# Kernel tuning notes

Measured on AMD Instinct MI355X. Metric: run time of the kernel, lower is better.

## Reference

```python
import jax, jax.numpy as jnp
import numpy as np

B, S, D, H, Dh = 2, 1024, 2048, 16, 128
EPS = 1e-6


def setup_inputs() -> dict:
    key = jax.random.key(0)
    ks = jax.random.split(key, 8)
    hidden_states = jax.random.normal(ks[0], (B, S, D), jnp.float32)
    def qweight(k):
        return jax.random.randint(k, (D, D), -127, 128, dtype=jnp.int32)
    wq, wk, wv, wo = qweight(ks[1]), qweight(ks[2]), qweight(ks[3]), qweight(ks[4])
    def scale(k):
        # per-output-channel dequant scale ~ O(1/(127*sqrt(D)))
        return jax.random.uniform(k, (D,), jnp.float32, 0.5, 1.5) / (127.0 * np.sqrt(D))
    wq_s, wk_s, wv_s, wo_s = scale(ks[5]), scale(ks[6]), scale(ks[7]), scale(jax.random.fold_in(key, 99))
    qn_w = jnp.ones((D,), jnp.float32)
    kn_w = jnp.ones((D,), jnp.float32)
    # RoPE tables (rotate-half convention): [S, Dh]
    pos = jnp.arange(S, dtype=jnp.float32)
    inv_freq = 1.0 / (10000.0 ** (jnp.arange(0, Dh, 2, dtype=jnp.float32) / Dh))
    freqs = pos[:, None] * inv_freq[None, :]              # [S, Dh/2]
    cos = jnp.concatenate([jnp.cos(freqs)] * 2, axis=-1)  # [S, Dh]
    sin = jnp.concatenate([jnp.sin(freqs)] * 2, axis=-1)
    lengths = jnp.array([S, 3 * S // 4], dtype=jnp.int32)
    return dict(hidden_states=hidden_states, wq_s=wq_s, wk_s=wk_s, wv_s=wv_s,
                wo_s=wo_s, qn_w=qn_w, kn_w=kn_w, cos=cos, sin=sin,
                wq=wq, wk=wk, wv=wv, wo=wo, lengths=lengths)


def _q8_linear(x, w_int, scale):
    # Q8Linear: int8 weight [out,in] dequantized by per-output-channel scale
    w = w_int.astype(jnp.float32) * scale[:, None]
    return jnp.einsum('bsd,od->bso', x, w)


def _rms_norm(x, w):
    var = jnp.mean(jnp.square(x), axis=-1, keepdims=True)
    return x * jax.lax.rsqrt(var + EPS) * w


def _apply_rope(x, cos, sin):
    # x: [B,S,D] -> per-head rotate-half RoPE -> [B,S,D]
    xh = x.reshape(B, S, H, Dh)
    x1, x2 = jnp.split(xh, 2, axis=-1)
    rot = jnp.concatenate([-x2, x1], axis=-1)
    out = xh * cos[None, :, None, :] + rot * sin[None, :, None, :]
    return out.reshape(B, S, D)


def reference(hidden_states, wq_s, wk_s, wv_s, wo_s, qn_w, kn_w, cos, sin,
              wq, wk, wv, wo, lengths):
    q = _rms_norm(_q8_linear(hidden_states, wq, wq_s), qn_w)
    k = _rms_norm(_q8_linear(hidden_states, wk, wk_s), kn_w)
    v = _q8_linear(hidden_states, wv, wv_s)
    q = _apply_rope(q, cos, sin)
    k = _apply_rope(k, cos, sin)
    # [B,S,D] -> [B,H,S,Dh]
    q = q.reshape(B, S, H, Dh).transpose(0, 2, 1, 3)
    k = k.reshape(B, S, H, Dh).transpose(0, 2, 1, 3)
    v = v.reshape(B, S, H, Dh).transpose(0, 2, 1, 3)
    # length mask -> additive bias [B,1,1,S]
    positions = jnp.arange(S)
    valid = positions[None, :] < lengths[:, None]
    bias = jnp.where(valid, 0.0, -jnp.inf).astype(jnp.float32)[:, None, None, :]
    scores = jnp.einsum('bhqd,bhkd->bhqk', q, k) / np.sqrt(Dh) + bias
    probs = jax.nn.softmax(scores, axis=-1)
    attn = jnp.einsum('bhqk,bhkd->bhqd', probs, v)
    attn = attn.transpose(0, 2, 1, 3).reshape(B, S, D)
    out = _q8_linear(attn, wo, wo_s)
    return out
```

## Files before the change

### kernel.cpp

```cpp
#include <hip/hip_runtime.h>
#include <stdint.h>

typedef __bf16 bf16;
typedef bf16 bf16x8 __attribute__((ext_vector_type(8)));
typedef bf16 bf16x4 __attribute__((ext_vector_type(4)));
typedef float f32x4 __attribute__((ext_vector_type(4)));

#define B_   2
#define S_   1024
#define D_   2048
#define H_   16
#define DH_  128
#define M_   (B_*S_)
#define EPSF 1e-6f

__device__ __forceinline__ void gload_lds16(const void* g, void* l) {
    __builtin_amdgcn_global_load_lds(
        (const __attribute__((address_space(1))) void*)g,
        (__attribute__((address_space(3))) void*)l,
        16, 0, 0);
}

struct ConvArgs {
    const void* s[5];
    bf16* d[5];
};

__global__ __launch_bounds__(256) void conv_all(ConvArgs a, int n) {
    const int z = blockIdx.y;
    const int i = (blockIdx.x * 256 + threadIdx.x) * 8;
    if (i + 8 > n) return;
    bf16x8 o;
    if (z == 0) {
        const float* src = (const float*)a.s[0];
        float4 v0 = *(const float4*)(src + i);
        float4 v1 = *(const float4*)(src + i + 4);
        o[0] = (bf16)v0.x; o[1] = (bf16)v0.y; o[2] = (bf16)v0.z; o[3] = (bf16)v0.w;
        o[4] = (bf16)v1.x; o[5] = (bf16)v1.y; o[6] = (bf16)v1.z; o[7] = (bf16)v1.w;
    } else {
        const int* src = (const int*)a.s[z];
        int4 v0 = *(const int4*)(src + i);
        int4 v1 = *(const int4*)(src + i + 4);
        o[0] = (bf16)(float)v0.x; o[1] = (bf16)(float)v0.y;
        o[2] = (bf16)(float)v0.z; o[3] = (bf16)(float)v0.w;
        o[4] = (bf16)(float)v1.x; o[5] = (bf16)(float)v1.y;
        o[6] = (bf16)(float)v1.z; o[7] = (bf16)(float)v1.w;
    }
    *(bf16x8*)(a.d[z] + i) = o;
}

struct GemmArgs {
    const bf16* W[3];
    const float* Sc[3];
    void* O[3];
    int mode[3];
};

__global__ __launch_bounds__(512, 2) void gemm8p(const bf16* __restrict__ A, GemmArgs args) {
    __shared__ char lds[131072];
    constexpr int NT = D_ / 64;

    const int z = blockIdx.z;
    const bf16* __restrict__ Wz = args.W[z];
    const float* __restrict__ Sc = args.Sc[z];
    const int mode = args.mode[z];
    const int t = threadIdx.x;
    const int w = t >> 6, l = t & 63;
    const int wr = w >> 2, wc = w & 3;
    const int m0 = blockIdx.y * 256, n0 = blockIdx.x * 256;
    const int hi = l >> 4, lo = l & 15;

    const int r8 = l >> 3;
    const int ce = ((l & 7) ^ (r8 & 7)) * 8;
    const bf16* Ag = A  + (size_t)(m0 + w * 8 + r8) * D_ + ce;
    const bf16* Bg = Wz + (size_t)(n0 + w * 8 + r8) * D_ + ce;

    auto stage = [&](int kt, int q) {
        if (kt >= NT) return;
        const bf16* g = (q < 2 ? Ag : Bg) + (size_t)((q & 1) * 128) * D_ + (size_t)kt * 64;
        char* d = lds + ((kt & 1) ? 65536 : 0) + q * 16384 + w * 1024;
        gload_lds16((const void*)g, (void*)d);
        gload_lds16((const void*)(g + (size_t)64 * D_), (void*)(d + 8192));
    };

    f32x4 acc[8][4] = {};

    stage(0, 0); stage(0, 1); stage(0, 2); stage(0, 3);
    stage(1, 2); stage(1, 0);
    asm volatile("s_waitcnt vmcnt(4)" ::: "memory");
    asm volatile("s_barrier" ::: "memory");

    for (int kt = 0; kt < NT; ++kt) {
        const char* Pb = lds + ((kt & 1) ? 65536 : 0);
        const char* As = Pb;
        const char* Bs = Pb + 32768;
        bf16x8 a[4][2], b01[2][2], b23[2][2];

        auto rdA = [&](int mi, int kk) -> bf16x8 {
            int row = wr * 128 + mi * 16 + lo;
            return *(const bf16x8*)(As + row * 128 + ((kk * 64 + hi * 16) ^ ((row & 7) << 4)));
        };
        auto rdB = [&](int ni, int kk) -> bf16x8 {
            int row = wc * 64 + ni * 16 + lo;
            return *(const bf16x8*)(Bs + row * 128 + ((kk * 64 + hi * 16) ^ ((row & 7) << 4)));
        };

#pragma unroll
        for (int mi = 0; mi < 4; ++mi) { a[mi][0] = rdA(mi, 0); a[mi][1] = rdA(mi, 1); }
#pragma unroll
        for (int ni = 0; ni < 2; ++ni) { b01[ni][0] = rdB(ni, 0); b01[ni][1] = rdB(ni, 1); }
        stage(kt + 1, 1);
        asm volatile("s_barrier" ::: "memory");
        asm volatile("s_waitcnt lgkmcnt(0)" ::: "memory");
        __builtin_amdgcn_sched_barrier(0);
        __builtin_amdgcn_s_setprio(1);
#pragma unroll
        for (int mi = 0; mi < 4; ++mi)
#pragma unroll
            for (int ni = 0; ni < 2; ++ni)
#pragma unroll
                for (int kk = 0; kk < 2; ++kk)
                    acc[mi][ni] = __builtin_amdgcn_mfma_f32_16x16x32_bf16(a[mi][kk], b01[ni][kk], acc[mi][ni], 0, 0, 0);
        __builtin_amdgcn_s_setprio(0);
        asm volatile("s_barrier" ::: "memory");

#pragma unroll
        for (int ni = 0; ni < 2; ++ni) { b23[ni][0] = rdB(2 + ni, 0); b23[ni][1] = rdB(2 + ni, 1); }
        stage(kt + 1, 3);
        asm volatile("s_barrier" ::: "memory");
        asm volatile("s_waitcnt lgkmcnt(0)" ::: "memory");
        __builtin_amdgcn_sched_barrier(0);
        __builtin_amdgcn_s_setprio(1);
#pragma unroll
        for (int mi = 0; mi < 4; ++mi)
#pragma unroll
            for (int ni = 0; ni < 2; ++ni)
#pragma unroll
                for (int kk = 0; kk < 2; ++kk)
                    acc[mi][2 + ni] = __builtin_amdgcn_mfma_f32_16x16x32_bf16(a[mi][kk], b23[ni][kk], acc[mi][2 + ni], 0, 0, 0);
        __builtin_amdgcn_s_setprio(0);
        asm volatile("s_barrier" ::: "memory");

#pragma unroll
        for (int mi = 0; mi < 4; ++mi) { a[mi][0] = rdA(4 + mi, 0); a[mi][1] = rdA(4 + mi, 1); }
        stage(kt + 2, 2);
        asm volatile("s_barrier" ::: "memory");
        asm volatile("s_waitcnt lgkmcnt(0)" ::: "memory");
        __builtin_amdgcn_sched_barrier(0);
        __builtin_amdgcn_s_setprio(1);
#pragma unroll
        for (int mi = 0; mi < 4; ++mi)
#pragma unroll
            for (int ni = 0; ni < 2; ++ni)
#pragma unroll
                for (int kk = 0; kk < 2; ++kk)
                    acc[4 + mi][2 + ni] = __builtin_amdgcn_mfma_f32_16x16x32_bf16(a[mi][kk], b23[ni][kk], acc[4 + mi][2 + ni], 0, 0, 0);
        __builtin_amdgcn_s_setprio(0);
        asm volatile("s_barrier" ::: "memory");

        stage(kt + 2, 0);
        asm volatile("s_barrier" ::: "memory");
        __builtin_amdgcn_sched_barrier(0);
        __builtin_amdgcn_s_setprio(1);
#pragma unroll
        for (int mi = 0; mi < 4; ++mi)
#pragma unroll
            for (int ni = 0; ni < 2; ++ni)
#pragma unroll
                for (int kk = 0; kk < 2; ++kk)
                    acc[4 + mi][ni] = __builtin_amdgcn_mfma_f32_16x16x32_bf16(a[mi][kk], b01[ni][kk], acc[4 + mi][ni], 0, 0, 0);
        __builtin_amdgcn_s_setprio(0);
        if (kt < NT - 2) asm volatile("s_waitcnt vmcnt(4)" ::: "memory");
        else             asm volatile("s_waitcnt vmcnt(0)" ::: "memory");
        asm volatile("s_barrier" ::: "memory");
    }

#pragma unroll
    for (int ni = 0; ni < 4; ++ni) {
        const int n = n0 + wc * 64 + ni * 16 + lo;
        const float scv = Sc[n];
#pragma unroll
        for (int mi = 0; mi < 8; ++mi) {
            const int mb = m0 + wr * 128 + mi * 16 + hi * 4;
            if (mode == 1) {
                bf16x4 pk;
#pragma unroll
                for (int r = 0; r < 4; ++r) pk[r] = (bf16)(acc[mi][ni][r] * scv);
                const int bb = mb >> 10, s = mb & 1023, hh = n >> 7, dh = n & 127;
                *(bf16x4*)(((bf16*)args.O[z]) + (((size_t)(bb * H_ + hh)) * DH_ + dh) * S_ + s) = pk;
            } else {
#pragma unroll
                for (int r = 0; r < 4; ++r)
                    ((bf16*)args.O[z])[(size_t)(mb + r) * D_ + n] = (bf16)(acc[mi][ni][r] * scv);
            }
        }
    }
}

__global__ __launch_bounds__(256, 2) void gemmO(const bf16* __restrict__ A, const bf16* __restrict__ W,
                                                const float* __restrict__ Sc, float* __restrict__ O) {
    __shared__ char lds[65536];
    constexpr int NT = D_ / 64;
    const int t = threadIdx.x;
    const int w = t >> 6, l = t & 63;
    const int wr = w >> 1, wc = w & 1;
    const int m0 = blockIdx.y * 128, n0 = blockIdx.x * 128;
    const int hi = l >> 4, lo = l & 15;

    const int r8 = l >> 3;
    const int ce = ((l & 7) ^ (r8 & 7)) * 8;
    const bf16* Ag = A + (size_t)(m0 + w * 8 + r8) * D_ + ce;
    const bf16* Bg = W + (size_t)(n0 + w * 8 + r8) * D_ + ce;

    auto stage = [&](int kt) {
        char* d = lds + (kt & 1) * 32768 + w * 1024;
        const bf16* ga = Ag + (size_t)kt * 64;
        const bf16* gb = Bg + (size_t)kt * 64;
#pragma unroll
        for (int j = 0; j < 4; ++j) {
            gload_lds16((const void*)(ga + (size_t)j * 32 * D_), (void*)(d + j * 4096));
            gload_lds16((const void*)(gb + (size_t)j * 32 * D_), (void*)(d + 16384 + j * 4096));
        }
    };

    f32x4 acc[4][4] = {};
    stage(0);
    for (int kt = 0; kt < NT; ++kt) {
        const char* cur = lds + (kt & 1) * 32768;
        if (kt + 1 < NT) {
            stage(kt + 1);
            asm volatile("s_waitcnt vmcnt(8)" ::: "memory");
        } else {
            asm volatile("s_waitcnt vmcnt(0)" ::: "memory");
        }
        asm volatile("s_barrier" ::: "memory");

        bf16x8 a[4][2], b[4][2];
#pragma unroll
        for (int mi = 0; mi < 4; ++mi)
#pragma unroll
            for (int kk = 0; kk < 2; ++kk) {
                int row = wr * 64 + mi * 16 + lo;
                a[mi][kk] = *(const bf16x8*)(cur + row * 128 + ((kk * 64 + hi * 16) ^ ((row & 7) << 4)));
            }
#pragma unroll
        for (int ni = 0; ni < 4; ++ni)
#pragma unroll
            for (int kk = 0; kk < 2; ++kk) {
                int row = wc * 64 + ni * 16 + lo;
                b[ni][kk] = *(const bf16x8*)(cur + 16384 + row * 128 + ((kk * 64 + hi * 16) ^ ((row & 7) << 4)));
            }
        __builtin_amdgcn_s_setprio(1);
#pragma unroll
        for (int mi = 0; mi < 4; ++mi)
#pragma unroll
            for (int ni = 0; ni < 4; ++ni)
#pragma unroll
                for (int kk = 0; kk < 2; ++kk)
                    acc[mi][ni] = __builtin_amdgcn_mfma_f32_16x16x32_bf16(a[mi][kk], b[ni][kk], acc[mi][ni], 0, 0, 0);
        __builtin_amdgcn_s_setprio(0);
        asm volatile("s_barrier" ::: "memory");
    }

#pragma unroll
    for (int ni = 0; ni < 4; ++ni) {
        const int n = n0 + wc * 64 + ni * 16 + lo;
        const float scv = Sc[n];
#pragma unroll
        for (int mi = 0; mi < 4; ++mi) {
            const int mb = m0 + wr * 64 + mi * 16 + hi * 4;
#pragma unroll
            for (int r = 0; r < 4; ++r)
                O[(size_t)(mb + r) * D_ + n] = acc[mi][ni][r] * scv;
        }
    }
}

__global__ __launch_bounds__(256) void rope_norm(const bf16* __restrict__ qr, const bf16* __restrict__ kr,
                                                 const float* __restrict__ qn, const float* __restrict__ kn,
                                                 const float* __restrict__ cosT, const float* __restrict__ sinT,
                                                 bf16* __restrict__ qOut, bf16* __restrict__ kOut) {
    const int which = blockIdx.z;
    const bf16* src = which ? kr : qr;
    const float* nw = which ? kn : qn;
    bf16* dst = which ? kOut : qOut;
    const int row = blockIdx.x;
    const int b = row >> 10, s = row & 1023;
    const int t = threadIdx.x;
    __shared__ float xs[D_];
    __shared__ float red[4];

    bf16x8 v = *(const bf16x8*)(src + (size_t)row * D_ + t * 8);
    float x[8]; float ss = 0.f;
#pragma unroll
    for (int j = 0; j < 8; ++j) { x[j] = (float)v[j]; ss += x[j] * x[j]; xs[t * 8 + j] = x[j]; }
#pragma unroll
    for (int msk = 32; msk; msk >>= 1) ss += __shfl_xor(ss, msk, 64);
    if ((t & 63) == 0) red[t >> 6] = ss;
    __syncthreads();
    const float inv = rsqrtf((red[0] + red[1] + red[2] + red[3]) / (float)D_ + EPSF);

    const int h = t >> 4;
    const int dh0 = (t & 15) * 8;
    bf16x8 o;
#pragma unroll
    for (int j = 0; j < 8; ++j) {
        int dd = dh0 + j;
        int d = h * 128 + dd;
        int pd = (dd < 64) ? d + 64 : d - 64;
        float xn = x[j] * inv * nw[d];
        float xp = xs[pd] * inv * nw[pd];
        float rot = (dd < 64) ? -xp : xp;
        o[j] = (bf16)(xn * cosT[s * DH_ + dd] + rot * sinT[s * DH_ + dd]);
    }
    *(bf16x8*)(dst + (((size_t)(b * H_ + h)) * S_ + s) * DH_ + dh0) = o;
}

__global__ __launch_bounds__(256) void flash(const bf16* __restrict__ Q, const bf16* __restrict__ Kb,
                                             const bf16* __restrict__ VTb, const int* __restrict__ lengths,
                                             bf16* __restrict__ Out) {
    __shared__ bf16 Qs[64 * 128];
    __shared__ bf16 Ks[64 * 128];
    __shared__ bf16 Vt[128 * 64];
    __shared__ bf16 Ps[4][16 * 64];
    const int t = threadIdx.x, w = t >> 6, l = t & 63;
    const int bh = blockIdx.y;
    const int b = bh >> 4;
    const int q0 = blockIdx.x * 64;
    const int L = lengths[b];
    const size_t base = (size_t)bh * S_ * DH_;
    const size_t vbase = (size_t)bh * DH_ * S_;
    const int hi = l >> 4, lo = l & 15;
    const int swz = (lo & 7) << 3;

    {
        const bf16* src = Q + base + (size_t)q0 * DH_;
#pragma unroll
        for (int i = 0; i < 4; ++i) {
            int r = (w * 4 + i) * 4 + (l >> 4);
            int sb = ((l & 15) * 16) ^ ((r & 7) << 4);
            gload_lds16((const void*)(src + (size_t)r * DH_ + (sb >> 1)), (void*)(Qs + (w * 4 + i) * 512));
        }
    }

    f32x4 O[8] = {};
    float mrow[4], lrow[4];
#pragma unroll
    for (int r = 0; r < 4; ++r) { mrow[r] = -1e30f; lrow[r] = 0.f; }
    const int nt = (L + 63) >> 6;
    const float sscale = 0.08838834764831843f;

    for (int kt = 0; kt < nt; ++kt) {
        const int k0 = kt * 64;
        __syncthreads();
        {
            const bf16* ksrc = Kb + base + (size_t)k0 * DH_;
#pragma unroll
            for (int i = 0; i < 4; ++i) {
                int r = (w * 4 + i) * 4 + (l >> 4);
                int sb = ((l & 15) * 16) ^ ((r & 7) << 4);
                gload_lds16((const void*)(ksrc + (size_t)r * DH_ + (sb >> 1)), (void*)(Ks + (w * 4 + i) * 512));
            }
        }
        {
            const bf16* vsrc = VTb + vbase + k0;
#pragma unroll
            for (int i = 0; i < 4; ++i) {
                int d = (w * 4 + i) * 8 + (l >> 3);
                int sb = ((l & 7) * 16) ^ ((d & 7) << 4);
                gload_lds16((const void*)(vsrc + (size_t)d * S_ + (sb >> 1)), (void*)(Vt + (w * 4 + i) * 512));
            }
        }
        __syncthreads();

        f32x4 sc[4] = {};
#pragma unroll
        for (int kk = 0; kk < 4; ++kk) {
            const int ko = kk * 32 + hi * 8;
            bf16x8 aq = *(const bf16x8*)(Qs + (w * 16 + lo) * 128 + (ko ^ swz));
#pragma unroll
            for (int ni = 0; ni < 4; ++ni) {
                bf16x8 bk = *(const bf16x8*)(Ks + (ni * 16 + lo) * 128 + (ko ^ swz));
                sc[ni] = __builtin_amdgcn_mfma_f32_16x16x32_bf16(aq, bk, sc[ni], 0, 0, 0);
            }
        }

        float p[4][4];
#pragma unroll
        for (int r = 0; r < 4; ++r) {
            float sv[4]; float vmax = -1e30f;
#pragma unroll
            for (int ni = 0; ni < 4; ++ni) {
                int kg = k0 + ni * 16 + lo;
                float vv = sc[ni][r] * sscale;
                if (kg >= L) vv = -1e30f;
                sv[ni] = vv;
                vmax = fmaxf(vmax, vv);
            }
#pragma unroll
            for (int msk = 1; msk < 16; msk <<= 1) vmax = fmaxf(vmax, __shfl_xor(vmax, msk, 64));
            float mnew = fmaxf(mrow[r], vmax);
            float corr = __expf(mrow[r] - mnew);
            float rs = 0.f;
#pragma unroll
            for (int ni = 0; ni < 4; ++ni) { float pv = __expf(sv[ni] - mnew); p[r][ni] = pv; rs += pv; }
#pragma unroll
            for (int msk = 1; msk < 16; msk <<= 1) rs += __shfl_xor(rs, msk, 64);
            lrow[r] = lrow[r] * corr + rs;
            mrow[r] = mnew;
#pragma unroll
            for (int di = 0; di < 8; ++di) O[di][r] *= corr;
        }

#pragma unroll
        for (int r = 0; r < 4; ++r) {
            int prow = hi * 4 + r;
#pragma unroll
            for (int ni = 0; ni < 4; ++ni)
                Ps[w][prow * 64 + (((ni * 16 + lo)) ^ ((prow & 7) << 3))] = (bf16)p[r][ni];
        }

#pragma unroll
        for (int kk = 0; kk < 2; ++kk) {
            const int ko = kk * 32 + hi * 8;
            bf16x8 ap = *(const bf16x8*)(&Ps[w][lo * 64 + (ko ^ swz)]);
#pragma unroll
            for (int di = 0; di < 8; ++di) {
                bf16x8 bv = *(const bf16x8*)(Vt + (di * 16 + lo) * 64 + (ko ^ swz));
                O[di] = __builtin_amdgcn_mfma_f32_16x16x32_bf16(ap, bv, O[di], 0, 0, 0);
            }
        }
    }

    const int h = bh & 15;
#pragma unroll
    for (int r = 0; r < 4; ++r) {
        float invl = 1.0f / lrow[r];
        int qrow = q0 + w * 16 + hi * 4 + r;
        bf16* orow = Out + (size_t)(b * S_ + qrow) * D_ + h * DH_;
#pragma unroll
        for (int di = 0; di < 8; ++di)
            orow[di * 16 + lo] = (bf16)(O[di][r] * invl);
    }
}

extern "C" void kernel_launch(void* const* d_in, const int* in_sizes, int n_in,
                              void* d_out, int out_size, void* d_ws, size_t ws_size,
                              hipStream_t stream) {
    const float* x    = (const float*)d_in[0];
    const float* wq_s = (const float*)d_in[1];
    const float* wk_s = (const float*)d_in[2];
    const float* wv_s = (const float*)d_in[3];
    const float* wo_s = (const float*)d_in[4];
    const float* qn   = (const float*)d_in[5];
    const float* kn   = (const float*)d_in[6];
    const float* cosT = (const float*)d_in[7];
    const float* sinT = (const float*)d_in[8];
    const int* wq = (const int*)d_in[9];
    const int* wk = (const int*)d_in[10];
    const int* wv = (const int*)d_in[11];
    const int* wo = (const int*)d_in[12];
    const int* lengths = (const int*)d_in[13];
    float* out = (float*)d_out;

    char* ws = (char*)d_ws;
    const size_t SLOT = (size_t)M_ * D_ * sizeof(bf16);
    bf16* xb   = (bf16*)(ws);
    bf16* wqb  = (bf16*)(ws + 1 * SLOT);
    bf16* wkb  = (bf16*)(ws + 2 * SLOT);
    bf16* wvb  = (bf16*)(ws + 3 * SLOT);
    bf16* wob  = (bf16*)(ws + 4 * SLOT);
    bf16* qr   = (bf16*)(ws + 5 * SLOT);
    bf16* kr   = (bf16*)(ws + 6 * SLOT);
    bf16* qb2  = (bf16*)(ws + 7 * SLOT);
    bf16* kb2  = (bf16*)(ws + 8 * SLOT);
    bf16* vb2  = (bf16*)(ws + 9 * SLOT);
    bf16* attnb = qr;

    const int NW = D_ * D_;
    ConvArgs ca;
    ca.s[0] = x;  ca.d[0] = xb;
    ca.s[1] = wq; ca.d[1] = wqb;
    ca.s[2] = wk; ca.d[2] = wkb;
    ca.s[3] = wv; ca.d[3] = wvb;
    ca.s[4] = wo; ca.d[4] = wob;
    conv_all<<<dim3(NW / 2048, 5), dim3(256), 0, stream>>>(ca, NW);

    GemmArgs ga;
    ga.W[0] = wqb; ga.W[1] = wkb; ga.W[2] = wvb;
    ga.Sc[0] = wq_s; ga.Sc[1] = wk_s; ga.Sc[2] = wv_s;
    ga.O[0] = qr; ga.O[1] = kr; ga.O[2] = vb2;
    ga.mode[0] = 2; ga.mode[1] = 2; ga.mode[2] = 1;
    gemm8p<<<dim3(D_ / 256, M_ / 256, 3), dim3(512), 0, stream>>>(xb, ga);

    rope_norm<<<dim3(M_, 1, 2), dim3(256), 0, stream>>>(qr, kr, qn, kn, cosT, sinT, qb2, kb2);

    flash<<<dim3(S_ / 64, B_ * H_, 1), dim3(256), 0, stream>>>(qb2, kb2, vb2, lengths, attnb);

    gemmO<<<dim3(D_ / 128, M_ / 128), dim3(256), 0, stream>>>(attnb, wob, wo_s, out);
}
```

Baseline: 155.8 us.

## Overlap Wo conversion with QKV GEMM and remap GEMM tiles per XCD

Moves the int32-to-bf16 conversion of the output-projection weight out of the standalone conversion kernel and into extra z=3 blocks of the QKV GEMM launch, so that conversion can run alongside the GEMM tiles instead of lengthening the memory-bound conversion pass. Both GEMM kernels also remap block IDs so that blocks dispatched to the same XCD (round-robin by block index) work on a compact 2D patch of output tiles, meant to improve L2 reuse of A and B panels. The extra blocks reserve the large LDS allocation even though they do not use it, and the mapping assumes the fixed grid shape.

```diff
diff --git a/kernel.cpp b/kernel.cpp
--- a/kernel.cpp
+++ b/kernel.cpp
@@ -22,8 +22,8 @@
 }
 
 struct ConvArgs {
-    const void* s[5];
-    bf16* d[5];
+    const void* s[4];
+    bf16* d[4];
 };
 
 __global__ __launch_bounds__(256) void conv_all(ConvArgs a, int n) {
@@ -54,20 +54,45 @@
     const float* Sc[3];
     void* O[3];
     int mode[3];
+    const int* wo_src;
+    bf16* wo_dst;
 };
 
 __global__ __launch_bounds__(512, 2) void gemm8p(const bf16* __restrict__ A, GemmArgs args) {
     __shared__ char lds[131072];
     constexpr int NT = D_ / 64;
-
     const int z = blockIdx.z;
+    const int t = threadIdx.x;
+
+    if (z == 3) {
+        const int flat = blockIdx.y * 8 + blockIdx.x;
+        const int* src = args.wo_src + (size_t)flat * 65536;
+        bf16* dst = args.wo_dst + (size_t)flat * 65536;
+#pragma unroll
+        for (int it = 0; it < 16; ++it) {
+            int off = it * 4096 + t * 8;
+            int4 v0 = *(const int4*)(src + off);
+            int4 v1 = *(const int4*)(src + off + 4);
+            bf16x8 o;
+            o[0] = (bf16)(float)v0.x; o[1] = (bf16)(float)v0.y;
+            o[2] = (bf16)(float)v0.z; o[3] = (bf16)(float)v0.w;
+            o[4] = (bf16)(float)v1.x; o[5] = (bf16)(float)v1.y;
+            o[6] = (bf16)(float)v1.z; o[7] = (bf16)(float)v1.w;
+            *(bf16x8*)(dst + off) = o;
+        }
+        return;
+    }
+
     const bf16* __restrict__ Wz = args.W[z];
     const float* __restrict__ Sc = args.Sc[z];
     const int mode = args.mode[z];
-    const int t = threadIdx.x;
     const int w = t >> 6, l = t & 63;
     const int wr = w >> 2, wc = w & 3;
-    const int m0 = blockIdx.y * 256, n0 = blockIdx.x * 256;
+    const int fid = blockIdx.x + 8 * blockIdx.y;
+    const int xcd = fid & 7, lid = fid >> 3;
+    const int tx = (xcd & 1) * 4 + (lid & 3);
+    const int ty = (xcd >> 1) * 2 + (lid >> 2);
+    const int m0 = ty * 256, n0 = tx * 256;
     const int hi = l >> 4, lo = l & 15;
 
     const int r8 = l >> 3;
@@ -204,7 +229,11 @@
     const int t = threadIdx.x;
     const int w = t >> 6, l = t & 63;
     const int wr = w >> 1, wc = w & 1;
-    const int m0 = blockIdx.y * 128, n0 = blockIdx.x * 128;
+    const int fid = blockIdx.x + 16 * blockIdx.y;
+    const int xcd = fid & 7, lid = fid >> 3;
+    const int tx = (xcd & 3) * 4 + (lid & 3);
+    const int ty = (xcd >> 2) * 8 + (lid >> 2);
+    const int m0 = ty * 128, n0 = tx * 128;
     const int hi = l >> 4, lo = l & 15;
 
     const int r8 = l >> 3;
@@ -483,15 +512,15 @@
     ca.s[1] = wq; ca.d[1] = wqb;
     ca.s[2] = wk; ca.d[2] = wkb;
     ca.s[3] = wv; ca.d[3] = wvb;
-    ca.s[4] = wo; ca.d[4] = wob;
-    conv_all<<<dim3(NW / 2048, 5), dim3(256), 0, stream>>>(ca, NW);
+    conv_all<<<dim3(NW / 2048, 4), dim3(256), 0, stream>>>(ca, NW);
 
     GemmArgs ga;
     ga.W[0] = wqb; ga.W[1] = wkb; ga.W[2] = wvb;
     ga.Sc[0] = wq_s; ga.Sc[1] = wk_s; ga.Sc[2] = wv_s;
     ga.O[0] = qr; ga.O[1] = kr; ga.O[2] = vb2;
     ga.mode[0] = 2; ga.mode[1] = 2; ga.mode[2] = 1;
-    gemm8p<<<dim3(D_ / 256, M_ / 256, 3), dim3(512), 0, stream>>>(xb, ga);
+    ga.wo_src = wo; ga.wo_dst = wob;
+    gemm8p<<<dim3(D_ / 256, M_ / 256, 4), dim3(512), 0, stream>>>(xb, ga);
 
     rope_norm<<<dim3(M_, 1, 2), dim3(256), 0, stream>>>(qr, kr, qn, kn, cosT, sinT, qb2, kb2);
 
```

After: 153.7 us. About the same (-1.3%).

## Fuse QKV GEMM over concatenated weights with 256x192 tiles to fill CUs

Applied to the files above, without the earlier changes.

Replaces the three-slice (blockIdx.z) QKV GEMM using 256x256 tiles with a single GEMM over the concatenated Q/K/V weight rows, using 256x192 output tiles. The grid grows from 192 to 256 blocks, so every CU gets work instead of leaving part of the machine idle in a single partial wave. The B tile now loads three 64-row chunks per stage and the waits are rebalanced. The epilogue works out per column which of Q, K or V it belongs to, because tiles straddle the 2048-column boundaries. This relies on the bf16 weight buffers being contiguous in the workspace.

```diff
diff --git a/kernel.cpp b/kernel.cpp
--- a/kernel.cpp
+++ b/kernel.cpp
@@ -49,67 +49,70 @@
     *(bf16x8*)(a.d[z] + i) = o;
 }
 
-struct GemmArgs {
-    const bf16* W[3];
+struct QKVArgs {
     const float* Sc[3];
-    void* O[3];
-    int mode[3];
+    bf16* qO; bf16* kO; bf16* vO;
 };
 
-__global__ __launch_bounds__(512, 2) void gemm8p(const bf16* __restrict__ A, GemmArgs args) {
-    __shared__ char lds[131072];
+__global__ __launch_bounds__(512, 2) void gemmQKV(const bf16* __restrict__ A, const bf16* __restrict__ Wcat,
+                                                  QKVArgs args) {
+    __shared__ char lds[114688];
     constexpr int NT = D_ / 64;
-
-    const int z = blockIdx.z;
-    const bf16* __restrict__ Wz = args.W[z];
-    const float* __restrict__ Sc = args.Sc[z];
-    const int mode = args.mode[z];
+    constexpr int BUF = 57344;
     const int t = threadIdx.x;
     const int w = t >> 6, l = t & 63;
     const int wr = w >> 2, wc = w & 3;
-    const int m0 = blockIdx.y * 256, n0 = blockIdx.x * 256;
+    const int m0 = blockIdx.y * 256, n0 = blockIdx.x * 192;
     const int hi = l >> 4, lo = l & 15;
 
     const int r8 = l >> 3;
     const int ce = ((l & 7) ^ (r8 & 7)) * 8;
-    const bf16* Ag = A  + (size_t)(m0 + w * 8 + r8) * D_ + ce;
-    const bf16* Bg = Wz + (size_t)(n0 + w * 8 + r8) * D_ + ce;
-
-    auto stage = [&](int kt, int q) {
+    const bf16* Ag = A    + (size_t)(m0 + w * 8 + r8) * D_ + ce;
+    const bf16* Bg = Wcat + (size_t)(n0 + w * 8 + r8) * D_ + ce;
+
+    auto stageA = [&](int kt, int half) {
         if (kt >= NT) return;
-        const bf16* g = (q < 2 ? Ag : Bg) + (size_t)((q & 1) * 128) * D_ + (size_t)kt * 64;
-        char* d = lds + ((kt & 1) ? 65536 : 0) + q * 16384 + w * 1024;
+        const bf16* g = Ag + (size_t)(half * 128) * D_ + (size_t)kt * 64;
+        char* d = lds + (kt & 1) * BUF + half * 16384 + w * 1024;
         gload_lds16((const void*)g, (void*)d);
         gload_lds16((const void*)(g + (size_t)64 * D_), (void*)(d + 8192));
     };
-
-    f32x4 acc[8][4] = {};
-
-    stage(0, 0); stage(0, 1); stage(0, 2); stage(0, 3);
-    stage(1, 2); stage(1, 0);
-    asm volatile("s_waitcnt vmcnt(4)" ::: "memory");
+    auto stageB = [&](int kt) {
+        if (kt >= NT) return;
+        const bf16* g = Bg + (size_t)kt * 64;
+        char* d = lds + (kt & 1) * BUF + 32768 + w * 1024;
+        gload_lds16((const void*)g, (void*)d);
+        gload_lds16((const void*)(g + (size_t)64 * D_), (void*)(d + 8192));
+        gload_lds16((const void*)(g + (size_t)128 * D_), (void*)(d + 16384));
+    };
+
+    f32x4 acc[8][3] = {};
+
+    stageA(0, 0); stageA(0, 1); stageB(0);
+    stageB(1); stageA(1, 0);
+    asm volatile("s_waitcnt vmcnt(5)" ::: "memory");
     asm volatile("s_barrier" ::: "memory");
 
     for (int kt = 0; kt < NT; ++kt) {
-        const char* Pb = lds + ((kt & 1) ? 65536 : 0);
+        const char* Pb = lds + (kt & 1) * BUF;
         const char* As = Pb;
         const char* Bs = Pb + 32768;
-        bf16x8 a[4][2], b01[2][2], b23[2][2];
+        bf16x8 a[4][2], b0[2], b1[2], b2[2];
 
         auto rdA = [&](int mi, int kk) -> bf16x8 {
             int row = wr * 128 + mi * 16 + lo;
             return *(const bf16x8*)(As + row * 128 + ((kk * 64 + hi * 16) ^ ((row & 7) << 4)));
         };
         auto rdB = [&](int ni, int kk) -> bf16x8 {
-            int row = wc * 64 + ni * 16 + lo;
+            int row = wc * 48 + ni * 16 + lo;
             return *(const bf16x8*)(Bs + row * 128 + ((kk * 64 + hi * 16) ^ ((row & 7) << 4)));
         };
 
 #pragma unroll
         for (int mi = 0; mi < 4; ++mi) { a[mi][0] = rdA(mi, 0); a[mi][1] = rdA(mi, 1); }
-#pragma unroll
-        for (int ni = 0; ni < 2; ++ni) { b01[ni][0] = rdB(ni, 0); b01[ni][1] = rdB(ni, 1); }
-        stage(kt + 1, 1);
+        b0[0] = rdB(0, 0); b0[1] = rdB(0, 1);
+        b1[0] = rdB(1, 0); b1[1] = rdB(1, 1);
+        stageA(kt + 1, 1);
         asm volatile("s_barrier" ::: "memory");
         asm volatile("s_waitcnt lgkmcnt(0)" ::: "memory");
         __builtin_amdgcn_sched_barrier(0);
@@ -117,16 +120,14 @@
 #pragma unroll
         for (int mi = 0; mi < 4; ++mi)
 #pragma unroll
-            for (int ni = 0; ni < 2; ++ni)
-#pragma unroll
-                for (int kk = 0; kk < 2; ++kk)
-                    acc[mi][ni] = __builtin_amdgcn_mfma_f32_16x16x32_bf16(a[mi][kk], b01[ni][kk], acc[mi][ni], 0, 0, 0);
+            for (int kk = 0; kk < 2; ++kk) {
+                acc[mi][0] = __builtin_amdgcn_mfma_f32_16x16x32_bf16(a[mi][kk], b0[kk], acc[mi][0], 0, 0, 0);
+                acc[mi][1] = __builtin_amdgcn_mfma_f32_16x16x32_bf16(a[mi][kk], b1[kk], acc[mi][1], 0, 0, 0);
+            }
         __builtin_amdgcn_s_setprio(0);
         asm volatile("s_barrier" ::: "memory");
 
-#pragma unroll
-        for (int ni = 0; ni < 2; ++ni) { b23[ni][0] = rdB(2 + ni, 0); b23[ni][1] = rdB(2 + ni, 1); }
-        stage(kt + 1, 3);
+        b2[0] = rdB(2, 0); b2[1] = rdB(2, 1);
         asm volatile("s_barrier" ::: "memory");
         asm volatile("s_waitcnt lgkmcnt(0)" ::: "memory");
         __builtin_amdgcn_sched_barrier(0);
@@ -134,16 +135,14 @@
 #pragma unroll
         for (int mi = 0; mi < 4; ++mi)
 #pragma unroll
-            for (int ni = 0; ni < 2; ++ni)
-#pragma unroll
-                for (int kk = 0; kk < 2; ++kk)
-                    acc[mi][2 + ni] = __builtin_amdgcn_mfma_f32_16x16x32_bf16(a[mi][kk], b23[ni][kk], acc[mi][2 + ni], 0, 0, 0);
+            for (int kk = 0; kk < 2; ++kk)
+                acc[mi][2] = __builtin_amdgcn_mfma_f32_16x16x32_bf16(a[mi][kk], b2[kk], acc[mi][2], 0, 0, 0);
         __builtin_amdgcn_s_setprio(0);
         asm volatile("s_barrier" ::: "memory");
 
 #pragma unroll
         for (int mi = 0; mi < 4; ++mi) { a[mi][0] = rdA(4 + mi, 0); a[mi][1] = rdA(4 + mi, 1); }
-        stage(kt + 2, 2);
+        stageB(kt + 2);
         asm volatile("s_barrier" ::: "memory");
         asm volatile("s_waitcnt lgkmcnt(0)" ::: "memory");
         __builtin_amdgcn_sched_barrier(0);
@@ -151,47 +150,47 @@
 #pragma unroll
         for (int mi = 0; mi < 4; ++mi)
 #pragma unroll
-            for (int ni = 0; ni < 2; ++ni)
-#pragma unroll
-                for (int kk = 0; kk < 2; ++kk)
-                    acc[4 + mi][2 + ni] = __builtin_amdgcn_mfma_f32_16x16x32_bf16(a[mi][kk], b23[ni][kk], acc[4 + mi][2 + ni], 0, 0, 0);
+            for (int kk = 0; kk < 2; ++kk) {
+                acc[4 + mi][1] = __builtin_amdgcn_mfma_f32_16x16x32_bf16(a[mi][kk], b1[kk], acc[4 + mi][1], 0, 0, 0);
+                acc[4 + mi][2] = __builtin_amdgcn_mfma_f32_16x16x32_bf16(a[mi][kk], b2[kk], acc[4 + mi][2], 0, 0, 0);
+            }
         __builtin_amdgcn_s_setprio(0);
         asm volatile("s_barrier" ::: "memory");
 
-        stage(kt + 2, 0);
+        stageA(kt + 2, 0);
         asm volatile("s_barrier" ::: "memory");
         __builtin_amdgcn_sched_barrier(0);
         __builtin_amdgcn_s_setprio(1);
 #pragma unroll
         for (int mi = 0; mi < 4; ++mi)
 #pragma unroll
-            for (int ni = 0; ni < 2; ++ni)
-#pragma unroll
-                for (int kk = 0; kk < 2; ++kk)
-                    acc[4 + mi][ni] = __builtin_amdgcn_mfma_f32_16x16x32_bf16(a[mi][kk], b01[ni][kk], acc[4 + mi][ni], 0, 0, 0);
+            for (int kk = 0; kk < 2; ++kk)
+                acc[4 + mi][0] = __builtin_amdgcn_mfma_f32_16x16x32_bf16(a[mi][kk], b0[kk], acc[4 + mi][0], 0, 0, 0);
         __builtin_amdgcn_s_setprio(0);
-        if (kt < NT - 2) asm volatile("s_waitcnt vmcnt(4)" ::: "memory");
+        if (kt < NT - 2) asm volatile("s_waitcnt vmcnt(5)" ::: "memory");
         else             asm volatile("s_waitcnt vmcnt(0)" ::: "memory");
         asm volatile("s_barrier" ::: "memory");
     }
 
 #pragma unroll
-    for (int ni = 0; ni < 4; ++ni) {
-        const int n = n0 + wc * 64 + ni * 16 + lo;
-        const float scv = Sc[n];
+    for (int ni = 0; ni < 3; ++ni) {
+        const int n = n0 + wc * 48 + ni * 16 + lo;
+        const int z = n >> 11, col = n & 2047;
+        const float scv = args.Sc[z][col];
 #pragma unroll
         for (int mi = 0; mi < 8; ++mi) {
             const int mb = m0 + wr * 128 + mi * 16 + hi * 4;
-            if (mode == 1) {
+            if (z == 2) {
                 bf16x4 pk;
 #pragma unroll
                 for (int r = 0; r < 4; ++r) pk[r] = (bf16)(acc[mi][ni][r] * scv);
-                const int bb = mb >> 10, s = mb & 1023, hh = n >> 7, dh = n & 127;
-                *(bf16x4*)(((bf16*)args.O[z]) + (((size_t)(bb * H_ + hh)) * DH_ + dh) * S_ + s) = pk;
+                const int bb = mb >> 10, s = mb & 1023, hh = col >> 7, dh = col & 127;
+                *(bf16x4*)(args.vO + (((size_t)(bb * H_ + hh)) * DH_ + dh) * S_ + s) = pk;
             } else {
+                bf16* dst = (z == 0 ? args.qO : args.kO);
 #pragma unroll
                 for (int r = 0; r < 4; ++r)
-                    ((bf16*)args.O[z])[(size_t)(mb + r) * D_ + n] = (bf16)(acc[mi][ni][r] * scv);
+                    dst[(size_t)(mb + r) * D_ + col] = (bf16)(acc[mi][ni][r] * scv);
             }
         }
     }
@@ -486,12 +485,10 @@
     ca.s[4] = wo; ca.d[4] = wob;
     conv_all<<<dim3(NW / 2048, 5), dim3(256), 0, stream>>>(ca, NW);
 
-    GemmArgs ga;
-    ga.W[0] = wqb; ga.W[1] = wkb; ga.W[2] = wvb;
-    ga.Sc[0] = wq_s; ga.Sc[1] = wk_s; ga.Sc[2] = wv_s;
-    ga.O[0] = qr; ga.O[1] = kr; ga.O[2] = vb2;
-    ga.mode[0] = 2; ga.mode[1] = 2; ga.mode[2] = 1;
-    gemm8p<<<dim3(D_ / 256, M_ / 256, 3), dim3(512), 0, stream>>>(xb, ga);
+    QKVArgs qa;
+    qa.Sc[0] = wq_s; qa.Sc[1] = wk_s; qa.Sc[2] = wv_s;
+    qa.qO = qr; qa.kO = kr; qa.vO = vb2;
+    gemmQKV<<<dim3(3 * D_ / 192, M_ / 256), dim3(512), 0, stream>>>(xb, wqb, qa);
 
     rope_norm<<<dim3(M_, 1, 2), dim3(256), 0, stream>>>(qr, kr, qn, kn, cosT, sinT, qb2, kb2);
 
```

Result: faster. 148.7 us (-4.5%).
